# Kernel optimization log

Measured on AMD Instinct MI355X. Metric: run time of the kernel, lower is better.

The kernel has to match this reference:

```python
import jax, jax.numpy as jnp
import numpy as np


def setup_inputs() -> dict:
    key = jax.random.key(0)
    ks = jax.random.split(key, 6)
    B, H, W, C = 4, 56, 56, 256
    NH, K = 8, 7
    return {
        "x": jax.random.normal(ks[0], (B, H, W, C), dtype=jnp.float32),
        "w_qkv": jax.random.normal(ks[1], (C, 3 * C), dtype=jnp.float32) * 0.02,
        "b_qkv": jax.random.normal(ks[2], (3 * C,), dtype=jnp.float32) * 0.02,
        "rpb": jax.random.normal(ks[3], (NH, K * K), dtype=jnp.float32) * 0.02,
        "w_proj": jax.random.normal(ks[4], (C, C), dtype=jnp.float32) * 0.02,
        "b_proj": jax.random.normal(ks[5], (C,), dtype=jnp.float32) * 0.02,
    }


def _window_stack(xp, H, W, ks):
    # xp: (B, H+2p, W+2p, nh, hd) zero-padded map.
    # Returns (B, H, W, nh, ks*ks, hd): each pixel's ks x ks neighborhood,
    # row-major (h offset outer, w offset inner) to match torch unfold order.
    return jnp.stack(
        [xp[:, i:i + H, j:j + W] for i in range(ks) for j in range(ks)],
        axis=-2,
    )


def reference(x, w_qkv, b_qkv, rpb, w_proj, b_proj):
    B, H, W, C = x.shape
    nh, ks2 = rpb.shape
    ks = int(np.sqrt(ks2) + 0.5)  # 7
    hd = C // nh
    scale = hd ** -0.5
    pad = ks // 2  # dilation == 1

    qkv = (x @ w_qkv + b_qkv).reshape(B, H, W, 3, nh, hd)
    q = qkv[..., 0, :, :] * scale        # (B,H,W,nh,hd)
    k = qkv[..., 1, :, :]
    v = qkv[..., 2, :, :]

    pads = ((0, 0), (pad, pad), (pad, pad), (0, 0), (0, 0))
    kw = _window_stack(jnp.pad(k, pads), H, W, ks)  # (B,H,W,nh,ks2,hd)
    vw = _window_stack(jnp.pad(v, pads), H, W, ks)

    # scores over each pixel's ks*ks neighbors (zero-padded borders kept,
    # matching the torch reference), plus relative position bias.
    attn = jnp.einsum("bhwnd,bhwnkd->bhwnk", q, kw) + rpb[None, None, None]
    attn = jax.nn.softmax(attn, axis=-1)
    out = jnp.einsum("bhwnk,bhwnkd->bhwnd", attn, vw).reshape(B, H, W, C)
    return out @ w_proj + b_proj
```

## Files before the change

kernel.cpp:

```cpp
#include <hip/hip_runtime.h>
#include <hip/hip_bf16.h>


using frag_ab = __attribute__((ext_vector_type(8))) short;
using f32x4   = __attribute__((ext_vector_type(4))) float;
using f32x2   = __attribute__((ext_vector_type(2))) float;

typedef const __attribute__((address_space(1))) unsigned int* gas_u32;
typedef __attribute__((address_space(3))) unsigned int*       las_u32;

__device__ __forceinline__ void gl_lds16(const void* g, void* l) {
    __builtin_amdgcn_global_load_lds((gas_u32)g, (las_u32)l, 16, 0, 0);
}

__device__ __forceinline__ float bflo(unsigned int u) { return __uint_as_float(u << 16); }
__device__ __forceinline__ float bfhi(unsigned int u) { return __uint_as_float(u & 0xffff0000u); }

__device__ __forceinline__ f32x2 unpk2(unsigned int u) {
    f32x2 r; r.x = bflo(u); r.y = bfhi(u); return r;
}

#if defined(__has_builtin)
#if __has_builtin(__builtin_amdgcn_fdot2_f32_bf16)
#define HAVE_FDOT2_BF16 1
#endif
#endif

#ifdef HAVE_FDOT2_BF16
typedef __bf16 bf16x2 __attribute__((ext_vector_type(2)));
__device__ __forceinline__ float dot2bf(unsigned int a, unsigned int b, float c) {
    union { unsigned int u; bf16x2 h; } ua, ub;
    ua.u = a; ub.u = b;
    return __builtin_amdgcn_fdot2_f32_bf16(ua.h, ub.h, c, false);
}
#endif

__global__ __launch_bounds__(256) void prep(
    const float* __restrict__ x,      __hip_bfloat16* __restrict__ xb,
    const float* __restrict__ w_qkv,  __hip_bfloat16* __restrict__ wqkvT,
    const float* __restrict__ w_proj, __hip_bfloat16* __restrict__ wprojT,
    __hip_bfloat16* __restrict__ kp,  __hip_bfloat16* __restrict__ vp)
{
    const int bid = blockIdx.x;
    const int tid = threadIdx.x;
    if (bid < 3136) {
        const int i = bid * 256 + tid;
        const float4 v = ((const float4*)x)[i];
        union { ushort4 u; __hip_bfloat16 h[4]; } o;
        o.h[0] = __float2bfloat16(v.x); o.h[1] = __float2bfloat16(v.y);
        o.h[2] = __float2bfloat16(v.z); o.h[3] = __float2bfloat16(v.w);
        ((ushort4*)xb)[i] = o.u;
    } else if (bid < 3904) {
        const int idx = (bid - 3136) * 256 + tid;
        const int k = idx & 255, n = idx >> 8;
        wqkvT[idx] = __float2bfloat16(w_qkv[k * 768 + n]);
    } else if (bid < 4160) {
        const int idx = (bid - 3904) * 256 + tid;
        const int k = idx & 255, n = idx >> 8;
        wprojT[idx] = __float2bfloat16(w_proj[k * 256 + n]);
    } else {
        const int u    = (bid - 4160) * 256 + tid;
        const int ip   = u / 30720;
        const int rem  = u - ip * 30720;
        const int cloc = rem >> 5;
        const int q16  = rem & 31;
        const int img  = ip >> 1;
        __hip_bfloat16* base = (ip & 1) ? vp : kp;
        int prow, pcol;
        if (cloc < 512) {
            const int r8 = cloc >> 6;
            prow = (r8 < 3) ? r8 : r8 + 56;
            pcol = cloc & 63;
        } else {
            const int c2 = cloc - 512;
            prow = 3 + (c2 >> 3);
            const int cc = c2 & 7;
            pcol = (cc < 3) ? cc : cc + 56;
        }
        *(uint4*)(base + (((size_t)(img * 64 + prow)) * 64 + pcol) * 256 + q16 * 8) =
            make_uint4(0u, 0u, 0u, 0u);
    }
}

#define GEMM128_BODY(EPILOGUE)                                                  \
    constexpr int K = 256;                                                      \
    __shared__ frag_ab As[8][64];                                     \
    __shared__ frag_ab Bs[8][64];                                     \
    const int tid  = threadIdx.x;                                               \
    const int lane = tid & 63;                                                  \
    const int w    = tid >> 6;                                                  \
    const int wm   = w >> 1, wn = w & 1;                                        \
    const int m0 = blockIdx.y * 128;                                            \
    const int n0 = blockIdx.x * 128;                                            \
    const int lrow = lane & 15;                                                 \
    const int lk   = (lane >> 4) * 8;                                           \
    const __hip_bfloat16* gA0 = A  + (size_t)(m0 + (2*w+0)*16 + lrow) * K + lk; \
    const __hip_bfloat16* gA1 = A  + (size_t)(m0 + (2*w+1)*16 + lrow) * K + lk; \
    const __hip_bfloat16* gB0 = BT + (size_t)(n0 + (2*w+0)*16 + lrow) * K + lk; \
    const __hip_bfloat16* gB1 = BT + (size_t)(n0 + (2*w+1)*16 + lrow) * K + lk; \
    f32x4 acc[4][4] = {};                                                       \
    for (int k0 = 0; k0 < K; k0 += 32) {                                        \
        gl_lds16(gA0 + k0, &As[2*w+0][0]);                                      \
        gl_lds16(gA1 + k0, &As[2*w+1][0]);                                      \
        gl_lds16(gB0 + k0, &Bs[2*w+0][0]);                                      \
        gl_lds16(gB1 + k0, &Bs[2*w+1][0]);                                      \
        __syncthreads();                                                        \
        frag_ab af[4], bf[4];                                                   \
        _Pragma("unroll")                                                       \
        for (int i = 0; i < 4; ++i) { af[i] = As[wm*4+i][lane]; bf[i] = Bs[wn*4+i][lane]; } \
        _Pragma("unroll")                                                       \
        for (int i = 0; i < 4; ++i)                                             \
            _Pragma("unroll")                                                   \
            for (int j = 0; j < 4; ++j)                                         \
                acc[i][j] = __builtin_amdgcn_mfma_f32_16x16x32_bf16(af[i], bf[j], acc[i][j], 0, 0, 0); \
        __syncthreads();                                                        \
    }                                                                           \
    const int rbase = (lane >> 4) * 4;                                          \
    const int cbase = lane & 15;                                                \
    _Pragma("unroll")                                                           \
    for (int fi = 0; fi < 4; ++fi) {                                            \
        const int rm = m0 + wm * 64 + fi * 16 + rbase;                          \
        _Pragma("unroll")                                                       \
        for (int fj = 0; fj < 4; ++fj) {                                        \
            const int cn = n0 + wn * 64 + fj * 16 + cbase;                      \
            const float bv = bias[cn];                                          \
            _Pragma("unroll")                                                   \
            for (int r = 0; r < 4; ++r) {                                       \
                const int m = rm + r;                                           \
                const float val = acc[fi][fj][r] + bv;                          \
                EPILOGUE                                                        \
            }                                                                   \
        }                                                                       \
    }

__global__ __launch_bounds__(256) void gemm_qkv(
    const __hip_bfloat16* __restrict__ A,
    const __hip_bfloat16* __restrict__ BT,
    const float* __restrict__ bias,
    __hip_bfloat16* __restrict__ qf,
    __hip_bfloat16* __restrict__ kp,
    __hip_bfloat16* __restrict__ vp,
    float qscale)
{
    GEMM128_BODY({
        const int sel = cn >> 8;
        if (sel == 0) {
            qf[(size_t)m * 256 + cn] = __float2bfloat16(val * qscale);
        } else {
            const int c  = cn & 255;
            const int b  = m / 3136;
            const int r2 = m % 3136;
            const int yy = r2 / 56;
            const int xx = r2 % 56;
            __hip_bfloat16* dst = (sel == 1) ? kp : vp;
            dst[(((size_t)(b * 64 + yy + 3)) * 64 + (xx + 3)) * 256 + c] =
                __float2bfloat16(val);
        }
    })
}

__global__ __launch_bounds__(256) void gemm_proj(
    const __hip_bfloat16* __restrict__ A,
    const __hip_bfloat16* __restrict__ BT,
    const float* __restrict__ bias,
    float* __restrict__ C)
{
    constexpr int K = 256;
    __shared__ frag_ab As[4][64];
    __shared__ frag_ab Bs[4][64];

    const int tid  = threadIdx.x;
    const int lane = tid & 63;
    const int w    = tid >> 6;
    const int wm   = w >> 1, wn = w & 1;
    const int m0 = blockIdx.y * 64;
    const int n0 = blockIdx.x * 64;

    const int lrow = lane & 15;
    const int lk   = (lane >> 4) * 8;
    const __hip_bfloat16* gA = A  + (size_t)(m0 + w * 16 + lrow) * K + lk;
    const __hip_bfloat16* gB = BT + (size_t)(n0 + w * 16 + lrow) * K + lk;

    f32x4 acc[2][2] = {};

    for (int k0 = 0; k0 < K; k0 += 32) {
        gl_lds16(gA + k0, &As[w][0]);
        gl_lds16(gB + k0, &Bs[w][0]);
        __syncthreads();
        const frag_ab a0 = As[2 * wm + 0][lane];
        const frag_ab a1 = As[2 * wm + 1][lane];
        const frag_ab b0 = Bs[2 * wn + 0][lane];
        const frag_ab b1 = Bs[2 * wn + 1][lane];
        acc[0][0] = __builtin_amdgcn_mfma_f32_16x16x32_bf16(a0, b0, acc[0][0], 0, 0, 0);
        acc[0][1] = __builtin_amdgcn_mfma_f32_16x16x32_bf16(a0, b1, acc[0][1], 0, 0, 0);
        acc[1][0] = __builtin_amdgcn_mfma_f32_16x16x32_bf16(a1, b0, acc[1][0], 0, 0, 0);
        acc[1][1] = __builtin_amdgcn_mfma_f32_16x16x32_bf16(a1, b1, acc[1][1], 0, 0, 0);
        __syncthreads();
    }

    const int rbase = (lane >> 4) * 4;
    const int cbase = lane & 15;
    #pragma unroll
    for (int fi = 0; fi < 2; ++fi) {
        const int rm = m0 + wm * 32 + fi * 16 + rbase;
        #pragma unroll
        for (int fj = 0; fj < 2; ++fj) {
            const int cn = n0 + wn * 32 + fj * 16 + cbase;
            const float bv = bias[cn];
            #pragma unroll
            for (int r = 0; r < 4; ++r)
                C[(size_t)(rm + r) * 256 + cn] = acc[fi][fj][r] + bv;
        }
    }
}

__global__ __launch_bounds__(64) void na2d_attn12(
    const __hip_bfloat16* __restrict__ qf,
    const __hip_bfloat16* __restrict__ kp,
    const __hip_bfloat16* __restrict__ vp,
    const float* __restrict__ rpb,
    __hip_bfloat16* __restrict__ out)
{
    const int lane = threadIdx.x;
    const int q8   = lane & 3;
    const int h    = (lane >> 2) & 7;
    const int tl   = (lane >> 5) & 1;

    const int bid = blockIdx.x;
    const int seg = (bid & 7) * 784 + (bid >> 3);
    const int row = seg / 28;
    const int x0  = (seg % 28) * 2;
    const int b   = row / 56;
    const int y   = row % 56;
    const int t   = row * 56 + x0 + tl;
    const int prow0 = b * 64 + y;

    __shared__ __hip_bfloat16 kbuf[8 * 256];
    __shared__ float srpb[8 * 49];

    for (int i = lane; i < 8 * 49; i += 64) srpb[i] = rpb[i];
    __syncthreads();

    unsigned int qpk[4];
    {
        const uint4 qa = *(const uint4*)(qf + (size_t)t * 256 + h * 32 + q8 * 8);
        qpk[0] = qa.x; qpk[1] = qa.y; qpk[2] = qa.z; qpk[3] = qa.w;
    }
#ifndef HAVE_FDOT2_BF16
    f32x2 q2[4];
    #pragma unroll
    for (int i = 0; i < 4; ++i) q2[i] = unpk2(qpk[i]);
#endif

    const int wroff = lane * 16;
    const int rdoff = tl * 512 + h * 64 + q8 * 16;

#define GLOAD(plane, ky, d0, d1, d2, d3)                                        \
    do {                                                                        \
        const char* rb_ = (const char*)((plane) +                               \
            ((size_t)(prow0 + (ky)) * 64 + x0) * 256 + lane * 8);               \
        d0 = *(const uint4*)(rb_);                                              \
        d1 = *(const uint4*)(rb_ + 1024);                                       \
        d2 = *(const uint4*)(rb_ + 2048);                                       \
        d3 = *(const uint4*)(rb_ + 3072);                                       \
    } while (0)

#define LWRITE(buf, s0, s1, s2, s3)                                             \
    do {                                                                        \
        char* wb_ = (char*)(buf) + wroff;                                       \
        *(uint4*)(wb_)        = s0;                                             \
        *(uint4*)(wb_ + 1024) = s1;                                             \
        *(uint4*)(wb_ + 2048) = s2;                                             \
        *(uint4*)(wb_ + 3072) = s3;                                             \
    } while (0)

    const float* rp = &srpb[h * 49];
    float m = -1e30f, l = 0.f;
    f32x2 o2[4] = {};

    uint4 k0, k1, k2, k3;
    GLOAD(kp, 0, k0, k1, k2, k3);

    #pragma unroll 1
    for (int ky = 0; ky < 7; ++ky) {
        LWRITE(kbuf, k0, k1, k2, k3);
        const __hip_bfloat16* vrow = vp +
            ((size_t)(prow0 + ky) * 64 + x0 + tl) * 256 + h * 32 + q8 * 8;
        uint4 va[7];
        #pragma unroll
        for (int kx = 0; kx < 7; ++kx)
            va[kx] = *(const uint4*)(vrow + kx * 256);
        if (ky < 6) GLOAD(kp, ky + 1, k0, k1, k2, k3);
        float lg[7];
        #pragma unroll
        for (int kx = 0; kx < 7; ++kx) {
            const uint4 w0 = *(const uint4*)((const char*)kbuf + rdoff + kx * 512);
#ifdef HAVE_FDOT2_BF16
            float s = 0.f;
            s = dot2bf(qpk[0], w0.x, s);
            s = dot2bf(qpk[1], w0.y, s);
            s = dot2bf(qpk[2], w0.z, s);
            s = dot2bf(qpk[3], w0.w, s);
#else
            f32x2 s2 = {0.f, 0.f};
            s2 += q2[0] * unpk2(w0.x);
            s2 += q2[1] * unpk2(w0.y);
            s2 += q2[2] * unpk2(w0.z);
            s2 += q2[3] * unpk2(w0.w);
            const float s = s2.x + s2.y;
#endif
            lg[kx] = s;
        }
        #pragma unroll
        for (int kx = 0; kx < 7; ++kx) {
            lg[kx] += __shfl_xor(lg[kx], 1, 64);
            lg[kx] += __shfl_xor(lg[kx], 2, 64);
            lg[kx] += rp[ky * 7 + kx];
        }
        float rmax = lg[0];
        #pragma unroll
        for (int kx = 1; kx < 7; ++kx) rmax = fmaxf(rmax, lg[kx]);
        const float mnew  = fmaxf(m, rmax);
        const float alpha = __expf(m - mnew);
        m = mnew;
        l *= alpha;
        const f32x2 alpha2 = {alpha, alpha};
        #pragma unroll
        for (int i = 0; i < 4; ++i) o2[i] *= alpha2;
        #pragma unroll
        for (int kx = 0; kx < 7; ++kx) {
            const float pr = __expf(lg[kx] - mnew);
            l += pr;
            const f32x2 pr2 = {pr, pr};
            const uint4 w0 = va[kx];
            o2[0] += pr2 * unpk2(w0.x);
            o2[1] += pr2 * unpk2(w0.y);
            o2[2] += pr2 * unpk2(w0.z);
            o2[3] += pr2 * unpk2(w0.w);
        }
    }
#undef GLOAD
#undef LWRITE

    const float inv = 1.f / l;
    union { uint4 u; __hip_bfloat16 hh[8]; } ob;
    #pragma unroll
    for (int i = 0; i < 4; ++i) {
        ob.hh[2 * i + 0] = __float2bfloat16(o2[i].x * inv);
        ob.hh[2 * i + 1] = __float2bfloat16(o2[i].y * inv);
    }
    *(uint4*)(out + (size_t)t * 256 + h * 32 + q8 * 8) = ob.u;
}

extern "C" void kernel_launch(void* const* d_in, const int* in_sizes, int n_in,
                              void* d_out, int out_size, void* d_ws, size_t ws_size,
                              hipStream_t stream)
{
    const float* x      = (const float*)d_in[0];
    const float* w_qkv  = (const float*)d_in[1];
    const float* b_qkv  = (const float*)d_in[2];
    const float* rpb    = (const float*)d_in[3];
    const float* w_proj = (const float*)d_in[4];
    const float* b_proj = (const float*)d_in[5];
    float* out = (float*)d_out;

    const int M = 12544;

    char* wsp = (char*)d_ws;
    __hip_bfloat16* qf    = (__hip_bfloat16*)wsp; wsp += (size_t)M * 256 * 2;
    __hip_bfloat16* kp    = (__hip_bfloat16*)wsp; wsp += (size_t)4 * 64 * 64 * 256 * 2;
    __hip_bfloat16* vp    = (__hip_bfloat16*)wsp; wsp += (size_t)4 * 64 * 64 * 256 * 2;
    __hip_bfloat16* xb    = (__hip_bfloat16*)wsp; wsp += (size_t)M * 256 * 2;
    __hip_bfloat16* attnb = (__hip_bfloat16*)wsp; wsp += (size_t)M * 256 * 2;
    __hip_bfloat16* wqkvT = (__hip_bfloat16*)wsp; wsp += (size_t)768 * 256 * 2;
    __hip_bfloat16* wprojT= (__hip_bfloat16*)wsp; wsp += (size_t)256 * 256 * 2;

    const float scale = 0.17677669529663689f;

    prep<<<5120, 256, 0, stream>>>(x, xb, w_qkv, wqkvT, w_proj, wprojT, kp, vp);

    gemm_qkv<<<dim3(6, 98), 256, 0, stream>>>(xb, wqkvT, b_qkv, qf, kp, vp, scale);

    na2d_attn12<<<6272, 64, 0, stream>>>(qf, kp, vp, rpb, attnb);

    gemm_proj<<<dim3(4, 196), 256, 0, stream>>>(attnb, wprojT, b_proj, out);
}
```

Before: 133.3 us.

## Fuse all four stages into one persistent cooperative kernel with grid syncs

```diff
diff --git a/kernel.cpp b/kernel.cpp
--- a/kernel.cpp
+++ b/kernel.cpp
@@ -1,5 +1,8 @@
 #include <hip/hip_runtime.h>
 #include <hip/hip_bf16.h>
+#include <hip/hip_cooperative_groups.h>
+
+namespace cg = cooperative_groups;
 
 
 using frag_ab = __attribute__((ext_vector_type(8))) short;
@@ -35,14 +38,13 @@
 }
 #endif
 
-__global__ __launch_bounds__(256) void prep(
+
+__device__ __forceinline__ void prep_body(
+    int bid, int tid,
     const float* __restrict__ x,      __hip_bfloat16* __restrict__ xb,
     const float* __restrict__ w_qkv,  __hip_bfloat16* __restrict__ wqkvT,
-    const float* __restrict__ w_proj, __hip_bfloat16* __restrict__ wprojT,
-    __hip_bfloat16* __restrict__ kp,  __hip_bfloat16* __restrict__ vp)
-{
-    const int bid = blockIdx.x;
-    const int tid = threadIdx.x;
+    const float* __restrict__ w_proj, __hip_bfloat16* __restrict__ wprojT)
+{
     if (bid < 3136) {
         const int i = bid * 256 + tid;
         const float4 v = ((const float4*)x)[i];
@@ -54,86 +56,40 @@
         const int idx = (bid - 3136) * 256 + tid;
         const int k = idx & 255, n = idx >> 8;
         wqkvT[idx] = __float2bfloat16(w_qkv[k * 768 + n]);
-    } else if (bid < 4160) {
+    } else {
         const int idx = (bid - 3904) * 256 + tid;
         const int k = idx & 255, n = idx >> 8;
         wprojT[idx] = __float2bfloat16(w_proj[k * 256 + n]);
+    }
+}
+
+__device__ __forceinline__ void border_body(
+    int vb, int tid, __hip_bfloat16* __restrict__ kp, __hip_bfloat16* __restrict__ vp)
+{
+    const int u    = vb * 256 + tid;
+    const int ip   = u / 30720;
+    const int rem  = u - ip * 30720;
+    const int cloc = rem >> 5;
+    const int q16  = rem & 31;
+    const int img  = ip >> 1;
+    __hip_bfloat16* base = (ip & 1) ? vp : kp;
+    int prow, pcol;
+    if (cloc < 512) {
+        const int r8 = cloc >> 6;
+        prow = (r8 < 3) ? r8 : r8 + 56;
+        pcol = cloc & 63;
     } else {
-        const int u    = (bid - 4160) * 256 + tid;
-        const int ip   = u / 30720;
-        const int rem  = u - ip * 30720;
-        const int cloc = rem >> 5;
-        const int q16  = rem & 31;
-        const int img  = ip >> 1;
-        __hip_bfloat16* base = (ip & 1) ? vp : kp;
-        int prow, pcol;
-        if (cloc < 512) {
-            const int r8 = cloc >> 6;
-            prow = (r8 < 3) ? r8 : r8 + 56;
-            pcol = cloc & 63;
-        } else {
-            const int c2 = cloc - 512;
-            prow = 3 + (c2 >> 3);
-            const int cc = c2 & 7;
-            pcol = (cc < 3) ? cc : cc + 56;
-        }
-        *(uint4*)(base + (((size_t)(img * 64 + prow)) * 64 + pcol) * 256 + q16 * 8) =
-            make_uint4(0u, 0u, 0u, 0u);
-    }
-}
-
-#define GEMM128_BODY(EPILOGUE)                                                  \
-    constexpr int K = 256;                                                      \
-    __shared__ frag_ab As[8][64];                                     \
-    __shared__ frag_ab Bs[8][64];                                     \
-    const int tid  = threadIdx.x;                                               \
-    const int lane = tid & 63;                                                  \
-    const int w    = tid >> 6;                                                  \
-    const int wm   = w >> 1, wn = w & 1;                                        \
-    const int m0 = blockIdx.y * 128;                                            \
-    const int n0 = blockIdx.x * 128;                                            \
-    const int lrow = lane & 15;                                                 \
-    const int lk   = (lane >> 4) * 8;                                           \
-    const __hip_bfloat16* gA0 = A  + (size_t)(m0 + (2*w+0)*16 + lrow) * K + lk; \
-    const __hip_bfloat16* gA1 = A  + (size_t)(m0 + (2*w+1)*16 + lrow) * K + lk; \
-    const __hip_bfloat16* gB0 = BT + (size_t)(n0 + (2*w+0)*16 + lrow) * K + lk; \
-    const __hip_bfloat16* gB1 = BT + (size_t)(n0 + (2*w+1)*16 + lrow) * K + lk; \
-    f32x4 acc[4][4] = {};                                                       \
-    for (int k0 = 0; k0 < K; k0 += 32) {                                        \
-        gl_lds16(gA0 + k0, &As[2*w+0][0]);                                      \
-        gl_lds16(gA1 + k0, &As[2*w+1][0]);                                      \
-        gl_lds16(gB0 + k0, &Bs[2*w+0][0]);                                      \
-        gl_lds16(gB1 + k0, &Bs[2*w+1][0]);                                      \
-        __syncthreads();                                                        \
-        frag_ab af[4], bf[4];                                                   \
-        _Pragma("unroll")                                                       \
-        for (int i = 0; i < 4; ++i) { af[i] = As[wm*4+i][lane]; bf[i] = Bs[wn*4+i][lane]; } \
-        _Pragma("unroll")                                                       \
-        for (int i = 0; i < 4; ++i)                                             \
-            _Pragma("unroll")                                                   \
-            for (int j = 0; j < 4; ++j)                                         \
-                acc[i][j] = __builtin_amdgcn_mfma_f32_16x16x32_bf16(af[i], bf[j], acc[i][j], 0, 0, 0); \
-        __syncthreads();                                                        \
-    }                                                                           \
-    const int rbase = (lane >> 4) * 4;                                          \
-    const int cbase = lane & 15;                                                \
-    _Pragma("unroll")                                                           \
-    for (int fi = 0; fi < 4; ++fi) {                                            \
-        const int rm = m0 + wm * 64 + fi * 16 + rbase;                          \
-        _Pragma("unroll")                                                       \
-        for (int fj = 0; fj < 4; ++fj) {                                        \
-            const int cn = n0 + wn * 64 + fj * 16 + cbase;                      \
-            const float bv = bias[cn];                                          \
-            _Pragma("unroll")                                                   \
-            for (int r = 0; r < 4; ++r) {                                       \
-                const int m = rm + r;                                           \
-                const float val = acc[fi][fj][r] + bv;                          \
-                EPILOGUE                                                        \
-            }                                                                   \
-        }                                                                       \
-    }
-
-__global__ __launch_bounds__(256) void gemm_qkv(
+        const int c2 = cloc - 512;
+        prow = 3 + (c2 >> 3);
+        const int cc = c2 & 7;
+        pcol = (cc < 3) ? cc : cc + 56;
+    }
+    *(uint4*)(base + (((size_t)(img * 64 + prow)) * 64 + pcol) * 256 + q16 * 8) =
+        make_uint4(0u, 0u, 0u, 0u);
+}
+
+__device__ __forceinline__ void qkv_body(
+    frag_ab (*As)[64], frag_ab (*Bs)[64], int tid, int m0, int n0,
     const __hip_bfloat16* __restrict__ A,
     const __hip_bfloat16* __restrict__ BT,
     const float* __restrict__ bias,
@@ -142,47 +98,80 @@
     __hip_bfloat16* __restrict__ vp,
     float qscale)
 {
-    GEMM128_BODY({
-        const int sel = cn >> 8;
-        if (sel == 0) {
-            qf[(size_t)m * 256 + cn] = __float2bfloat16(val * qscale);
-        } else {
-            const int c  = cn & 255;
-            const int b  = m / 3136;
-            const int r2 = m % 3136;
-            const int yy = r2 / 56;
-            const int xx = r2 % 56;
-            __hip_bfloat16* dst = (sel == 1) ? kp : vp;
-            dst[(((size_t)(b * 64 + yy + 3)) * 64 + (xx + 3)) * 256 + c] =
-                __float2bfloat16(val);
-        }
-    })
-}
-
-__global__ __launch_bounds__(256) void gemm_proj(
+    constexpr int K = 256;
+    const int lane = tid & 63;
+    const int w    = tid >> 6;
+    const int wm   = w >> 1, wn = w & 1;
+    const int lrow = lane & 15;
+    const int lk   = (lane >> 4) * 8;
+    const __hip_bfloat16* gA0 = A  + (size_t)(m0 + (2*w+0)*16 + lrow) * K + lk;
+    const __hip_bfloat16* gA1 = A  + (size_t)(m0 + (2*w+1)*16 + lrow) * K + lk;
+    const __hip_bfloat16* gB0 = BT + (size_t)(n0 + (2*w+0)*16 + lrow) * K + lk;
+    const __hip_bfloat16* gB1 = BT + (size_t)(n0 + (2*w+1)*16 + lrow) * K + lk;
+    f32x4 acc[4][4] = {};
+    for (int k0 = 0; k0 < K; k0 += 32) {
+        gl_lds16(gA0 + k0, &As[2*w+0][0]);
+        gl_lds16(gA1 + k0, &As[2*w+1][0]);
+        gl_lds16(gB0 + k0, &Bs[2*w+0][0]);
+        gl_lds16(gB1 + k0, &Bs[2*w+1][0]);
+        __syncthreads();
+        frag_ab af[4], bf[4];
+        #pragma unroll
+        for (int i = 0; i < 4; ++i) { af[i] = As[wm*4+i][lane]; bf[i] = Bs[wn*4+i][lane]; }
+        #pragma unroll
+        for (int i = 0; i < 4; ++i)
+            #pragma unroll
+            for (int j = 0; j < 4; ++j)
+                acc[i][j] = __builtin_amdgcn_mfma_f32_16x16x32_bf16(af[i], bf[j], acc[i][j], 0, 0, 0);
+        __syncthreads();
+    }
+    const int rbase = (lane >> 4) * 4;
+    const int cbase = lane & 15;
+    #pragma unroll
+    for (int fi = 0; fi < 4; ++fi) {
+        const int rm = m0 + wm * 64 + fi * 16 + rbase;
+        #pragma unroll
+        for (int fj = 0; fj < 4; ++fj) {
+            const int cn = n0 + wn * 64 + fj * 16 + cbase;
+            const float bv = bias[cn];
+            #pragma unroll
+            for (int r = 0; r < 4; ++r) {
+                const int mm  = rm + r;
+                const float val = acc[fi][fj][r] + bv;
+                const int sel = cn >> 8;
+                if (sel == 0) {
+                    qf[(size_t)mm * 256 + cn] = __float2bfloat16(val * qscale);
+                } else {
+                    const int c  = cn & 255;
+                    const int bb = mm / 3136;
+                    const int r2 = mm % 3136;
+                    const int yy = r2 / 56;
+                    const int xx = r2 % 56;
+                    __hip_bfloat16* dst = (sel == 1) ? kp : vp;
+                    dst[(((size_t)(bb * 64 + yy + 3)) * 64 + (xx + 3)) * 256 + c] =
+                        __float2bfloat16(val);
+                }
+            }
+        }
+    }
+}
+
+__device__ __forceinline__ void proj_body(
+    frag_ab (*As)[64], frag_ab (*Bs)[64], int tid, int m0, int n0,
     const __hip_bfloat16* __restrict__ A,
     const __hip_bfloat16* __restrict__ BT,
     const float* __restrict__ bias,
     float* __restrict__ C)
 {
     constexpr int K = 256;
-    __shared__ frag_ab As[4][64];
-    __shared__ frag_ab Bs[4][64];
-
-    const int tid  = threadIdx.x;
     const int lane = tid & 63;
     const int w    = tid >> 6;
     const int wm   = w >> 1, wn = w & 1;
-    const int m0 = blockIdx.y * 64;
-    const int n0 = blockIdx.x * 64;
-
     const int lrow = lane & 15;
     const int lk   = (lane >> 4) * 8;
     const __hip_bfloat16* gA = A  + (size_t)(m0 + w * 16 + lrow) * K + lk;
     const __hip_bfloat16* gB = BT + (size_t)(n0 + w * 16 + lrow) * K + lk;
-
     f32x4 acc[2][2] = {};
-
     for (int k0 = 0; k0 < K; k0 += 32) {
         gl_lds16(gA + k0, &As[w][0]);
         gl_lds16(gB + k0, &Bs[w][0]);
@@ -197,7 +186,6 @@
         acc[1][1] = __builtin_amdgcn_mfma_f32_16x16x32_bf16(a1, b1, acc[1][1], 0, 0, 0);
         __syncthreads();
     }
-
     const int rbase = (lane >> 4) * 4;
     const int cbase = lane & 15;
     #pragma unroll
@@ -214,48 +202,7 @@
     }
 }
 
-__global__ __launch_bounds__(64) void na2d_attn12(
-    const __hip_bfloat16* __restrict__ qf,
-    const __hip_bfloat16* __restrict__ kp,
-    const __hip_bfloat16* __restrict__ vp,
-    const float* __restrict__ rpb,
-    __hip_bfloat16* __restrict__ out)
-{
-    const int lane = threadIdx.x;
-    const int q8   = lane & 3;
-    const int h    = (lane >> 2) & 7;
-    const int tl   = (lane >> 5) & 1;
-
-    const int bid = blockIdx.x;
-    const int seg = (bid & 7) * 784 + (bid >> 3);
-    const int row = seg / 28;
-    const int x0  = (seg % 28) * 2;
-    const int b   = row / 56;
-    const int y   = row % 56;
-    const int t   = row * 56 + x0 + tl;
-    const int prow0 = b * 64 + y;
-
-    __shared__ __hip_bfloat16 kbuf[8 * 256];
-    __shared__ float srpb[8 * 49];
-
-    for (int i = lane; i < 8 * 49; i += 64) srpb[i] = rpb[i];
-    __syncthreads();
-
-    unsigned int qpk[4];
-    {
-        const uint4 qa = *(const uint4*)(qf + (size_t)t * 256 + h * 32 + q8 * 8);
-        qpk[0] = qa.x; qpk[1] = qa.y; qpk[2] = qa.z; qpk[3] = qa.w;
-    }
-#ifndef HAVE_FDOT2_BF16
-    f32x2 q2[4];
-    #pragma unroll
-    for (int i = 0; i < 4; ++i) q2[i] = unpk2(qpk[i]);
-#endif
-
-    const int wroff = lane * 16;
-    const int rdoff = tl * 512 + h * 64 + q8 * 16;
-
-#define GLOAD(plane, ky, d0, d1, d2, d3)                                        \
+#define GLOAD4(plane, ky, d0, d1, d2, d3)                                       \
     do {                                                                        \
         const char* rb_ = (const char*)((plane) +                               \
             ((size_t)(prow0 + (ky)) * 64 + x0) * 256 + lane * 8);               \
@@ -265,7 +212,7 @@
         d3 = *(const uint4*)(rb_ + 3072);                                       \
     } while (0)
 
-#define LWRITE(buf, s0, s1, s2, s3)                                             \
+#define LWRITE4(buf, s0, s1, s2, s3)                                            \
     do {                                                                        \
         char* wb_ = (char*)(buf) + wroff;                                       \
         *(uint4*)(wb_)        = s0;                                             \
@@ -274,23 +221,55 @@
         *(uint4*)(wb_ + 3072) = s3;                                             \
     } while (0)
 
+__device__ __forceinline__ void attn_wave_body(
+    int lane, int seg, __hip_bfloat16* kbuf, const float* srpb,
+    const __hip_bfloat16* __restrict__ qf,
+    const __hip_bfloat16* __restrict__ kp,
+    const __hip_bfloat16* __restrict__ vp,
+    __hip_bfloat16* __restrict__ out)
+{
+    const int q8   = lane & 3;
+    const int h    = (lane >> 2) & 7;
+    const int tl   = (lane >> 5) & 1;
+
+    const int row = seg / 28;
+    const int x0  = (seg % 28) * 2;
+    const int b   = row / 56;
+    const int y   = row % 56;
+    const int t   = row * 56 + x0 + tl;
+    const int prow0 = b * 64 + y;
+
+    unsigned int qpk[4];
+    {
+        const uint4 qa = *(const uint4*)(qf + (size_t)t * 256 + h * 32 + q8 * 8);
+        qpk[0] = qa.x; qpk[1] = qa.y; qpk[2] = qa.z; qpk[3] = qa.w;
+    }
+#ifndef HAVE_FDOT2_BF16
+    f32x2 q2[4];
+    #pragma unroll
+    for (int i = 0; i < 4; ++i) q2[i] = unpk2(qpk[i]);
+#endif
+
+    const int wroff = lane * 16;
+    const int rdoff = tl * 512 + h * 64 + q8 * 16;
+
     const float* rp = &srpb[h * 49];
     float m = -1e30f, l = 0.f;
     f32x2 o2[4] = {};
 
     uint4 k0, k1, k2, k3;
-    GLOAD(kp, 0, k0, k1, k2, k3);
+    GLOAD4(kp, 0, k0, k1, k2, k3);
 
     #pragma unroll 1
     for (int ky = 0; ky < 7; ++ky) {
-        LWRITE(kbuf, k0, k1, k2, k3);
+        LWRITE4(kbuf, k0, k1, k2, k3);
         const __hip_bfloat16* vrow = vp +
             ((size_t)(prow0 + ky) * 64 + x0 + tl) * 256 + h * 32 + q8 * 8;
         uint4 va[7];
         #pragma unroll
         for (int kx = 0; kx < 7; ++kx)
             va[kx] = *(const uint4*)(vrow + kx * 256);
-        if (ky < 6) GLOAD(kp, ky + 1, k0, k1, k2, k3);
+        if (ky < 6) GLOAD4(kp, ky + 1, k0, k1, k2, k3);
         float lg[7];
         #pragma unroll
         for (int kx = 0; kx < 7; ++kx) {
@@ -339,8 +318,6 @@
             o2[3] += pr2 * unpk2(w0.w);
         }
     }
-#undef GLOAD
-#undef LWRITE
 
     const float inv = 1.f / l;
     union { uint4 u; __hip_bfloat16 hh[8]; } ob;
@@ -350,6 +327,108 @@
         ob.hh[2 * i + 1] = __float2bfloat16(o2[i].y * inv);
     }
     *(uint4*)(out + (size_t)t * 256 + h * 32 + q8 * 8) = ob.u;
+}
+
+#undef GLOAD4
+#undef LWRITE4
+
+struct FParams {
+    const float* x; const float* w_qkv; const float* b_qkv; const float* rpb;
+    const float* w_proj; const float* b_proj; float* out;
+    __hip_bfloat16 *xb, *qf, *kp, *vp, *attnb, *wqkvT, *wprojT;
+    float qscale;
+};
+
+__global__ __launch_bounds__(256) void fused_na2d(FParams p)
+{
+    __shared__ __align__(16) char smem[18432];
+    const int tid = threadIdx.x;
+    cg::grid_group grid = cg::this_grid();
+
+    for (int vb = blockIdx.x; vb < 4160; vb += gridDim.x)
+        prep_body(vb, tid, p.x, p.xb, p.w_qkv, p.wqkvT, p.w_proj, p.wprojT);
+    grid.sync();
+
+    {
+        frag_ab (*As)[64] = (frag_ab(*)[64])(smem);
+        frag_ab (*Bs)[64] = (frag_ab(*)[64])(smem + 8192);
+        for (int vb = blockIdx.x; vb < 1548; vb += gridDim.x) {
+            if (vb < 960) {
+                border_body(vb, tid, p.kp, p.vp);
+            } else {
+                const int vq = vb - 960;
+                qkv_body(As, Bs, tid, (vq / 6) * 128, (vq % 6) * 128,
+                         p.xb, p.wqkvT, p.b_qkv, p.qf, p.kp, p.vp, p.qscale);
+            }
+        }
+    }
+    grid.sync();
+
+    {
+        __hip_bfloat16* kbufw = (__hip_bfloat16*)(smem + (tid >> 6) * 4096);
+        float* srpb = (float*)(smem + 16384);
+        for (int i = tid; i < 8 * 49; i += 256) srpb[i] = p.rpb[i];
+        __syncthreads();
+        const int w = tid >> 6, lane = tid & 63;
+        for (int vg = blockIdx.x; vg < 1568; vg += gridDim.x) {
+            const int seg = (vg & 7) * 784 + (vg >> 3) * 4 + w;
+            attn_wave_body(lane, seg, kbufw, srpb, p.qf, p.kp, p.vp, p.attnb);
+        }
+    }
+    grid.sync();
+
+    {
+        frag_ab (*As)[64] = (frag_ab(*)[64])(smem);
+        frag_ab (*Bs)[64] = (frag_ab(*)[64])(smem + 4096);
+        for (int vb = blockIdx.x; vb < 784; vb += gridDim.x)
+            proj_body(As, Bs, tid, (vb >> 2) * 64, (vb & 3) * 64,
+                      p.attnb, p.wprojT, p.b_proj, p.out);
+    }
+}
+
+__global__ __launch_bounds__(256) void prep_k(
+    const float* __restrict__ x,      __hip_bfloat16* __restrict__ xb,
+    const float* __restrict__ w_qkv,  __hip_bfloat16* __restrict__ wqkvT,
+    const float* __restrict__ w_proj, __hip_bfloat16* __restrict__ wprojT,
+    __hip_bfloat16* __restrict__ kp,  __hip_bfloat16* __restrict__ vp)
+{
+    const int bid = blockIdx.x;
+    if (bid < 4160) prep_body(bid, threadIdx.x, x, xb, w_qkv, wqkvT, w_proj, wprojT);
+    else            border_body(bid - 4160, threadIdx.x, kp, vp);
+}
+
+__global__ __launch_bounds__(256) void gemm_qkv_k(
+    const __hip_bfloat16* __restrict__ A, const __hip_bfloat16* __restrict__ BT,
+    const float* __restrict__ bias, __hip_bfloat16* __restrict__ qf,
+    __hip_bfloat16* __restrict__ kp, __hip_bfloat16* __restrict__ vp, float qscale)
+{
+    __shared__ frag_ab As[8][64];
+    __shared__ frag_ab Bs[8][64];
+    qkv_body(As, Bs, threadIdx.x, blockIdx.y * 128, blockIdx.x * 128,
+             A, BT, bias, qf, kp, vp, qscale);
+}
+
+__global__ __launch_bounds__(256) void gemm_proj_k(
+    const __hip_bfloat16* __restrict__ A, const __hip_bfloat16* __restrict__ BT,
+    const float* __restrict__ bias, float* __restrict__ C)
+{
+    __shared__ frag_ab As[4][64];
+    __shared__ frag_ab Bs[4][64];
+    proj_body(As, Bs, threadIdx.x, blockIdx.y * 64, blockIdx.x * 64, A, BT, bias, C);
+}
+
+__global__ __launch_bounds__(64) void na2d_attn_k(
+    const __hip_bfloat16* __restrict__ qf, const __hip_bfloat16* __restrict__ kp,
+    const __hip_bfloat16* __restrict__ vp, const float* __restrict__ rpb,
+    __hip_bfloat16* __restrict__ out)
+{
+    __shared__ __hip_bfloat16 kbuf[8 * 256];
+    __shared__ float srpb[8 * 49];
+    for (int i = threadIdx.x; i < 8 * 49; i += 64) srpb[i] = rpb[i];
+    __syncthreads();
+    const int bid = blockIdx.x;
+    const int seg = (bid & 7) * 784 + (bid >> 3);
+    attn_wave_body(threadIdx.x, seg, kbuf, srpb, qf, kp, vp, out);
 }
 
 extern "C" void kernel_launch(void* const* d_in, const int* in_sizes, int n_in,
@@ -377,11 +456,39 @@
 
     const float scale = 0.17677669529663689f;
 
-    prep<<<5120, 256, 0, stream>>>(x, xb, w_qkv, wqkvT, w_proj, wprojT, kp, vp);
-
-    gemm_qkv<<<dim3(6, 98), 256, 0, stream>>>(xb, wqkvT, b_qkv, qf, kp, vp, scale);
-
-    na2d_attn12<<<6272, 64, 0, stream>>>(qf, kp, vp, rpb, attnb);
-
-    gemm_proj<<<dim3(4, 196), 256, 0, stream>>>(attnb, wprojT, b_proj, out);
-}
+    FParams p;
+    p.x = x; p.w_qkv = w_qkv; p.b_qkv = b_qkv; p.rpb = rpb;
+    p.w_proj = w_proj; p.b_proj = b_proj; p.out = out;
+    p.xb = xb; p.qf = qf; p.kp = kp; p.vp = vp; p.attnb = attnb;
+    p.wqkvT = wqkvT; p.wprojT = wprojT; p.qscale = scale;
+
+    static int coopGrid = 0;
+    static bool inited = false;
+    if (!inited) {
+        inited = true;
+        int dev = 0;
+        if (hipGetDevice(&dev) == hipSuccess) {
+            int sup = 0, ncu = 0, nb = 0;
+            hipDeviceGetAttribute(&sup, hipDeviceAttributeCooperativeLaunch, dev);
+            hipDeviceGetAttribute(&ncu, hipDeviceAttributeMultiprocessorCount, dev);
+            hipError_t e = hipOccupancyMaxActiveBlocksPerMultiprocessor(
+                &nb, (const void*)fused_na2d, 256, 0);
+            if (sup && e == hipSuccess && nb > 0 && ncu > 0)
+                coopGrid = nb * ncu;
+        }
+    }
+
+    if (coopGrid > 0) {
+        void* args[] = { (void*)&p };
+        hipError_t e = hipLaunchCooperativeKernel(
+            (const void*)fused_na2d, dim3(coopGrid), dim3(256), args, 0, stream);
+        if (e == hipSuccess) return;
+        (void)hipGetLastError();
+        coopGrid = 0;
+    }
+
+    prep_k<<<5120, 256, 0, stream>>>(x, xb, w_qkv, wqkvT, w_proj, wprojT, kp, vp);
+    gemm_qkv_k<<<dim3(6, 98), 256, 0, stream>>>(xb, wqkvT, b_qkv, qf, kp, vp, scale);
+    na2d_attn_k<<<6272, 64, 0, stream>>>(qf, kp, vp, rpb, attnb);
+    gemm_proj_k<<<dim3(4, 196), 256, 0, stream>>>(attnb, wprojT, b_proj, out);
+}
```

Result: slower. 269.5 us (+102.1%).
